# Kernel tuning notes

Measured on AMD Instinct MI355X. Metric: run time of the kernel, lower is better.

The kernel has to match this reference:

```python
import jax, jax.numpy as jnp
import numpy as np

B = 50000      # batch of graphs
NOBJ = 7       # tangram pieces per graph
HID = 64
EMB = 32
SIGMA = 25.0   # VE-SDE sigma for marginal_prob_std


def _lin_init(k, fin, fout):
    kw, kb = jax.random.split(k)
    s = 1.0 / np.sqrt(fin)
    w = jax.random.uniform(kw, (fin, fout), minval=-s, maxval=s, dtype=jnp.float32)
    b = jax.random.uniform(kb, (fout,), minval=-s, maxval=s, dtype=jnp.float32)
    return w, b


def setup_inputs() -> dict:
    key = jax.random.key(0)
    ks = jax.random.split(key, 16)
    N = B * NOBJ
    omega = jax.random.normal(ks[0], (N, 3), dtype=jnp.float32)
    t = jax.random.uniform(ks[1], (B, 1), minval=1e-3, maxval=1.0, dtype=jnp.float32)
    # fully-connected edges (no self loops) per graph, offset by graph index
    a, b = np.meshgrid(np.arange(NOBJ), np.arange(NOBJ), indexing='ij')
    m = a != b
    src0, dst0 = a[m], b[m]                       # (42,)
    offs = (np.arange(B) * NOBJ)[:, None]         # (B,1)
    src = (src0[None, :] + offs).reshape(-1)
    dst = (dst0[None, :] + offs).reshape(-1)
    edge_index = jnp.asarray(np.stack([src, dst]), dtype=jnp.int32)  # (2, B*42)
    W_fourier = jax.random.normal(ks[2], (EMB // 2,), dtype=jnp.float32) * 30.0
    wi1, bi1 = _lin_init(ks[3], 3, HID)
    wi2, bi2 = _lin_init(ks[4], HID, HID)
    wt, bt = _lin_init(ks[5], EMB, EMB)
    w1a, b1a = _lin_init(ks[6], HID * 2, HID)
    w1b, b1b = _lin_init(ks[7], HID, HID)
    w2a, b2a = _lin_init(ks[8], (HID + EMB) * 2, HID)
    w2b, b2b = _lin_init(ks[9], HID, HID)
    w3a, b3a = _lin_init(ks[10], (HID + EMB) * 2, HID)
    w3b, b3b = _lin_init(ks[11], HID, 3)
    return dict(omega=omega, edge_index=edge_index, t=t, num_objs=NOBJ,
                W_fourier=W_fourier,
                wi1=wi1, bi1=bi1, wi2=wi2, bi2=bi2, wt=wt, bt=bt,
                w1a=w1a, b1a=b1a, w1b=w1b, b1b=b1b,
                w2a=w2a, b2a=b2a, w2b=w2b, b2b=b2b,
                w3a=w3a, b3a=b3a, w3b=w3b, b3b=b3b)


def _mlp(x, wa, ba, wb, bb):
    return jax.nn.relu(x @ wa + ba) @ wb + bb


def reference(omega, edge_index, t, num_objs, W_fourier,
              wi1, bi1, wi2, bi2, wt, bt,
              w1a, b1a, w1b, b1b, w2a, b2a, w2b, b2b, w3a, b3a, w3b, b3b):
    N = omega.shape[0]
    src, dst = edge_index[0], edge_index[1]

    def edge_conv(x, wa, ba, wb, bb):
        # EdgeConv: msg = mlp([x_i, x_j - x_i]); max-aggregate at target i
        xi = x[dst]
        msg = _mlp(jnp.concatenate([xi, x[src] - xi], axis=-1), wa, ba, wb, bb)
        return jax.ops.segment_max(msg, dst, num_segments=N)

    init_feature = _mlp(omega, wi1, bi1, wi2, bi2)          # (N, HID)
    # Gaussian Fourier time embedding -> ReLU -> Linear -> ReLU
    proj = t[:, 0][:, None] * W_fourier[None, :] * (2.0 * jnp.pi)   # (B, EMB/2)
    emb = jnp.concatenate([jnp.sin(proj), jnp.cos(proj)], axis=-1)  # (B, EMB)
    xs = jax.nn.relu(jax.nn.relu(emb) @ wt + bt)                    # (B, EMB)
    # torch: xs.repeat(1, num_objs, 1).view(B*num_objs, -1) == tile whole block
    x_sigma = jnp.tile(xs, (num_objs, 1))                           # (N, EMB)

    x = jax.nn.relu(edge_conv(init_feature, w1a, b1a, w1b, b1b))
    x = jnp.concatenate([x, x_sigma], axis=-1)
    x = jax.nn.relu(edge_conv(x, w2a, b2a, w2b, b2b))
    x = jnp.concatenate([x, x_sigma], axis=-1)
    x = edge_conv(x, w3a, b3a, w3b, b3b)                            # (N, 3)

    # torch: t.repeat(1, num_objs).view(B*num_objs, -1) == repeat_interleave
    t_r = jnp.repeat(t, num_objs, axis=0)                           # (N, 1)
    std = jnp.sqrt((SIGMA ** (2.0 * t_r) - 1.0) / (2.0 * jnp.log(SIGMA)))
    return x / (std + 1e-7)
```

## Files before the change

### kernel.cpp

```cpp
#include <hip/hip_runtime.h>


#define NB 50000

typedef unsigned short u16;
typedef unsigned int u32;
typedef short short8 __attribute__((ext_vector_type(8)));
typedef float f32x4 __attribute__((ext_vector_type(4)));

#define OFF_I  0
#define OFF_1A 8192
#define OFF_2A 24576
#define OFF_3A 49152
#define OFF_1B 73728
#define OFF_2B 81920
#define OFF_WT 90112
#define OFF_3B 92160

#define HSTR 144
#define HLO  2304
#define H2S  272
#define SSTR 264
#define WREG 8832

__device__ __forceinline__ float b2f(u16 u) {
    return __uint_as_float(((u32)u) << 16);
}
__device__ __forceinline__ u16 f2b(float f) {
    u32 u = __float_as_uint(f);
    u += 0x7FFFu + ((u >> 16) & 1u);
    return (u16)(u >> 16);
}
__device__ __forceinline__ void split2(float v, u16& h, u16& l) {
    u32 u = __float_as_uint(v);
    h = (u16)(u >> 16);
    float d = v - __uint_as_float(u & 0xffff0000u);
    l = f2b(d);
}
__device__ __forceinline__ u32 splitpack(float v) {
    u32 u = __float_as_uint(v);
    float d = v - __uint_as_float(u & 0xffff0000u);
    u32 r = __float_as_uint(d);
    r += 0x7FFFu + ((r >> 16) & 1u);
    return __builtin_amdgcn_perm(r, u, 0x07060302);
}
__device__ __forceinline__ float bcast(float v, int l) {
    return __uint_as_float(__builtin_amdgcn_readlane(__float_as_uint(v), l));
}

__global__ __launch_bounds__(128) void pack_kernel(
    const float* __restrict__ wi2, const float* __restrict__ w1a,
    const float* __restrict__ w2a, const float* __restrict__ w3a,
    const float* __restrict__ w1b, const float* __restrict__ w2b,
    const float* __restrict__ wt,  const float* __restrict__ w3b,
    u16* __restrict__ ws)
{
    int blk = blockIdx.x;
    int j    = blockIdx.y;
    int half = threadIdx.x >> 6;
    int lane = threadIdx.x & 63;
    float v;
    u16* dst;
    if (blk < 88) {
        const float* src; int NT, qoff, obase, frag;
        if (blk < 8)       { src = wi2; NT = 4; qoff = 0;  obase = OFF_I;  frag = blk;      }
        else if (blk < 24) { src = w1a; NT = 8; qoff = 64; obase = OFF_1A; frag = blk - 8;  }
        else if (blk < 48) { src = w2a; NT = 8; qoff = 96; obase = OFF_2A; frag = blk - 24; }
        else if (blk < 72) { src = w3a; NT = 8; qoff = 96; obase = OFF_3A; frag = blk - 48; }
        else if (blk < 80) { src = w1b; NT = 4; qoff = 0;  obase = OFF_1B; frag = blk - 72; }
        else               { src = w2b; NT = 4; qoff = 0;  obase = OFF_2B; frag = blk - 80; }
        int kt = frag / NT, nt = frag % NT;
        int k = kt * 32 + (lane >> 4) * 8 + j;
        int n = nt * 16 + (lane & 15);
        int idx = (n < 64) ? (k * 64 + n) : ((qoff + k) * 64 + (n - 64));
        v = src[idx];
        dst = ws + obase + frag * 1024 + half * 512 + lane * 8 + j;
    } else if (blk < 90) {
        int frag = blk - 88;
        int k = (lane >> 4) * 8 + j;
        int n = frag * 16 + (lane & 15);
        v = wt[k * 32 + n];
        dst = ws + OFF_WT + frag * 1024 + half * 512 + lane * 8 + j;
    } else {
        int frag = blk - 90;
        int k = frag * 32 + (lane >> 4) * 8 + j;
        int n = lane & 15;
        v = (n < 3) ? w3b[k * 3 + n] : 0.f;
        dst = ws + OFF_3B + frag * 1024 + half * 512 + lane * 8 + j;
    }
    u16 hi = f2b(v);
    *dst = (half == 0) ? hi : f2b(v - b2f(hi));
}

__device__ __forceinline__ f32x4 mfma1(short8 a, short8 b, f32x4 acc) {
    return __builtin_amdgcn_mfma_f32_16x16x32_bf16(a, b, acc, 0, 0, 0);
}
__device__ __forceinline__ f32x4 mfma3(short8 ah, short8 al, short8 bh, short8 bl, f32x4 acc) {
    acc = mfma1(ah, bh, acc);
    acc = mfma1(ah, bl, acc);
    acc = mfma1(al, bh, acc);
    return acc;
}

#define ROW(k) ((k) < 7 ? (k) : (k) + 1)

__device__ __forceinline__ void writeX64_14(char* G, int L, const float* v) {
#pragma unroll
    for (int k = 0; k < 14; ++k) {
        int r = ROW(k);
        u16 h, l;
        split2(v[k], h, l);
        *(u16*)(G + r * HSTR + L * 2) = h;
        *(u16*)(G + HLO + r * HSTR + L * 2) = l;
    }
}
__device__ __forceinline__ void loadA2(const char* G, int L, short8* Ah, short8* Al) {
#pragma unroll
    for (int kt = 0; kt < 2; ++kt) {
        Ah[kt] = *(const short8*)(G + (L & 15) * HSTR + kt * 64 + (L >> 4) * 16);
        Al[kt] = *(const short8*)(G + HLO + (L & 15) * HSTR + kt * 64 + (L >> 4) * 16);
    }
}
template<int KT, int NT>
__device__ __forceinline__ void lin_pass(const u16* __restrict__ ws, int off, int nt0,
                                         const short8* Ah, const short8* Al,
                                         char* Sg, int L) {
#pragma unroll
    for (int ntc = 0; ntc < 4; ++ntc) {
        f32x4 a1 = {0.f, 0.f, 0.f, 0.f}, a2 = {0.f, 0.f, 0.f, 0.f};
#pragma unroll
        for (int kt = 0; kt < KT; ++kt) {
            int f = kt * NT + nt0 + ntc;
            short8 bh = *(const short8*)(ws + off + f * 1024 + L * 8);
            short8 bl = *(const short8*)(ws + off + f * 1024 + 512 + L * 8);
            a1 = mfma1(Ah[kt], bh, a1);
            a2 = mfma1(Ah[kt], bl, a2);
            a2 = mfma1(Al[kt], bh, a2);
        }
#pragma unroll
        for (int rr = 0; rr < 4; ++rr)
            *(float*)(Sg + ((L >> 4) * 4 + rr) * SSTR + ntc * 64 + (L & 15) * 4) = a1[rr] + a2[rr];
    }
}
__device__ __forceinline__ void readS14(const char* Sg, int L, float* o) {
#pragma unroll
    for (int k = 0; k < 14; ++k) o[k] = *(const float*)(Sg + ROW(k) * SSTR + L * 4);
}
__device__ __forceinline__ void stageH2(char* G, int c, const float* pp, const float* qq, int L) {
#pragma unroll
    for (int r = 0; r < 16; ++r) {
        int e = c * 16 + r;
        if (e < 84) {
            int gb = (e >= 42) ? 1 : 0;
            int el = e - gb * 42;
            int i = el / 6, jj = el - i * 6;
            int j = jj + (jj >= i);
            float hv = fmaxf(pp[gb * 7 + i] + qq[gb * 7 + j], 0.f);
            *(u32*)(G + r * H2S + L * 4) = splitpack(hv);
        }
    }
}
__device__ __forceinline__ void unpack4(const uint4& a, u32* ho, u32* lo) {
    ho[0] = __builtin_amdgcn_perm(a.y, a.x, 0x05040100);
    ho[1] = __builtin_amdgcn_perm(a.w, a.z, 0x05040100);
    lo[0] = __builtin_amdgcn_perm(a.y, a.x, 0x07060302);
    lo[1] = __builtin_amdgcn_perm(a.w, a.z, 0x07060302);
}
__device__ __forceinline__ void loadAH(const char* G, int L,
                                       short8& Ah0, short8& Ah1, short8& Al0, short8& Al1) {
    const char* base = G + (L & 15) * H2S + (L >> 4) * 32;
    uint4 a0 = *(const uint4*)(base);
    uint4 a1 = *(const uint4*)(base + 16);
    uint4 b0 = *(const uint4*)(base + 128);
    uint4 b1 = *(const uint4*)(base + 144);
    union { u32 u[4]; short8 s; } h0, h1, l0, l1;
    unpack4(a0, &h0.u[0], &l0.u[0]);
    unpack4(a1, &h0.u[2], &l0.u[2]);
    unpack4(b0, &h1.u[0], &l1.u[0]);
    unpack4(b1, &h1.u[2], &l1.u[2]);
    Ah0 = h0.s; Al0 = l0.s; Ah1 = h1.s; Al1 = l1.s;
}
__device__ __forceinline__ void maxread(const char* Sb, int cc, float* mx, int L) {
#pragma unroll
    for (int r = 0; r < 16; ++r) {
        int e = cc * 16 + r;
        if (e < 84) {
            int gb = (e >= 42) ? 1 : 0;
            int i = (e - gb * 42) / 6;
            float sv = *(const float*)(Sb + r * SSTR + L * 4);
            mx[gb * 7 + i] = fmaxf(mx[gb * 7 + i], sv);
        }
    }
}

__device__ __forceinline__ void edgeconv_pipe(const u16* __restrict__ ws, int offB,
                                              char* W, char* Sb,
                                              const float* pp, const float* qq,
                                              float vb, int L) {
    float mx[14];
#pragma unroll
    for (int k = 0; k < 14; ++k) mx[k] = -3.0e38f;
    stageH2(W, 0, pp, qq, L);
    short8 Ah0, Ah1, Al0, Al1;
    loadAH(W, L, Ah0, Ah1, Al0, Al1);
#pragma unroll
    for (int c = 0; c < 6; ++c) {
        if (c < 5) stageH2(W, c + 1, pp, qq, L);
        if (c > 0) maxread(Sb, c - 1, mx, L);
#pragma unroll
        for (int nt = 0; nt < 4; ++nt) {
            short8 bh0 = *(const short8*)(ws + offB + nt * 1024 + L * 8);
            short8 bl0 = *(const short8*)(ws + offB + nt * 1024 + 512 + L * 8);
            short8 bh1 = *(const short8*)(ws + offB + (4 + nt) * 1024 + L * 8);
            short8 bl1 = *(const short8*)(ws + offB + (4 + nt) * 1024 + 512 + L * 8);
            f32x4 a1 = {0.f, 0.f, 0.f, 0.f}, a2 = {0.f, 0.f, 0.f, 0.f};
            a1 = mfma1(Ah0, bh0, a1);
            a2 = mfma1(Ah0, bl0, a2);
            a2 = mfma1(Al0, bh0, a2);
            a1 = mfma1(Ah1, bh1, a1);
            a2 = mfma1(Ah1, bl1, a2);
            a2 = mfma1(Al1, bh1, a2);
#pragma unroll
            for (int rr = 0; rr < 4; ++rr)
                *(float*)(Sb + ((L >> 4) * 4 + rr) * SSTR + nt * 64 + (L & 15) * 4) = a1[rr] + a2[rr];
        }
        if (c < 5) loadAH(W, L, Ah0, Ah1, Al0, Al1);
    }
    maxread(Sb, 5, mx, L);
    float xo[14];
#pragma unroll
    for (int k = 0; k < 14; ++k) xo[k] = fmaxf(mx[k] + vb, 0.f);
    writeX64_14(W, L, xo);
}

__global__ __launch_bounds__(128, 3) void gnn_kernel(
    const float* __restrict__ omega, const float* __restrict__ tt, const float* __restrict__ Wf,
    const float* __restrict__ wi1, const float* __restrict__ bi1, const float* __restrict__ bi2,
    const float* __restrict__ bt,
    const float* __restrict__ b1a, const float* __restrict__ b1b,
    const float* __restrict__ b2a, const float* __restrict__ b2b,
    const float* __restrict__ b3a, const float* __restrict__ b3b,
    const u16* __restrict__ ws, float* __restrict__ out)
{
    __shared__ __align__(16) char smem[2 * WREG];
    const int L   = threadIdx.x & 63;
    const int wav = threadIdx.x >> 6;
    const int p   = blockIdx.x * 2 + wav;
    const int g0  = p * 2;
    const int base0 = g0 * 7;
    char* W   = smem + wav * WREG;
    char* Sb  = W + 4608;

    float omv = (L < 42) ? omega[base0 * 3 + L] : 0.f;
    float vwi10 = wi1[L], vwi11 = wi1[64 + L], vwi12 = wi1[128 + L];
    float vbi1 = bi1[L];
    float h1[14];
#pragma unroll
    for (int k = 0; k < 14; ++k) {
        float a0 = bcast(omv, 3 * k), a1 = bcast(omv, 3 * k + 1), a2 = bcast(omv, 3 * k + 2);
        h1[k] = fmaxf(fmaf(a0, vwi10, fmaf(a1, vwi11, fmaf(a2, vwi12, vbi1))), 0.f);
    }

    short8 Ah2, Al2;
    {
        int cc = L & 31;
        float vwf = Wf[cc & 15] * 6.283185307179586f;
        int tb = base0 - (base0 / NB) * NB;
#pragma unroll
        for (int k = 0; k < 14; ++k) {
            int ti = tb + k; if (ti >= NB) ti -= NB;
            float pj = tt[ti] * vwf;
            float remb = fmaxf((cc < 16) ? __sinf(pj) : __cosf(pj), 0.f);
            u16 h, l;
            split2(remb, h, l);
            if (L < 32) *(u16*)(W + ROW(k) * HSTR + cc * 2) = h;
            else *(u16*)(W + HLO + ROW(k) * HSTR + cc * 2) = l;
        }
        short8 Eh = *(const short8*)(W + (L & 15) * HSTR + (L >> 4) * 16);
        short8 El = *(const short8*)(W + HLO + (L & 15) * HSTR + (L >> 4) * 16);
#pragma unroll
        for (int nt = 0; nt < 2; ++nt) {
            short8 bh = *(const short8*)(ws + OFF_WT + nt * 1024 + L * 8);
            short8 bl = *(const short8*)(ws + OFF_WT + nt * 1024 + 512 + L * 8);
            f32x4 acc = {0.f, 0.f, 0.f, 0.f};
            acc = mfma3(Eh, El, bh, bl, acc);
#pragma unroll
            for (int rr = 0; rr < 4; ++rr)
                *(float*)(Sb + ((L >> 4) * 4 + rr) * SSTR + nt * 64 + (L & 15) * 4) = acc[rr];
        }
        float vbt = bt[cc];
#pragma unroll
        for (int k = 0; k < 14; ++k) {
            float xv = fmaxf(*(const float*)(Sb + ROW(k) * SSTR + cc * 4) + vbt, 0.f);
            u16 h, l;
            split2(xv, h, l);
            if (L < 32) *(u16*)(W + ROW(k) * HSTR + cc * 2) = h;
            else *(u16*)(W + HLO + ROW(k) * HSTR + cc * 2) = l;
        }
        Ah2 = *(const short8*)(W + (L & 15) * HSTR + (L >> 4) * 16);
        Al2 = *(const short8*)(W + HLO + (L & 15) * HSTR + (L >> 4) * 16);
    }

    short8 Ah[3], Al[3];
    float pp[14], qq[14];

    writeX64_14(W, L, h1);
    loadA2(W, L, Ah, Al);
    lin_pass<2, 4>(ws, OFF_I, 0, Ah, Al, Sb, L);
    {
        float xh[14];
        readS14(Sb, L, xh);
        float vbi2 = bi2[L];
#pragma unroll
        for (int k = 0; k < 14; ++k) xh[k] += vbi2;
        writeX64_14(W, L, xh);
    }

    loadA2(W, L, Ah, Al);
    lin_pass<2, 8>(ws, OFF_1A, 0, Ah, Al, Sb, L);
    readS14(Sb, L, pp);
    lin_pass<2, 8>(ws, OFF_1A, 4, Ah, Al, Sb, L);
    readS14(Sb, L, qq);
    float vb1a = b1a[L];
#pragma unroll
    for (int k = 0; k < 14; ++k) pp[k] = pp[k] + vb1a - qq[k];
    edgeconv_pipe(ws, OFF_1B, W, Sb, pp, qq, b1b[L], L);

    loadA2(W, L, Ah, Al);
    Ah[2] = Ah2; Al[2] = Al2;
    lin_pass<3, 8>(ws, OFF_2A, 0, Ah, Al, Sb, L);
    readS14(Sb, L, pp);
    lin_pass<3, 8>(ws, OFF_2A, 4, Ah, Al, Sb, L);
    readS14(Sb, L, qq);
    float vb2a = b2a[L];
#pragma unroll
    for (int k = 0; k < 14; ++k) pp[k] = pp[k] + vb2a - qq[k];
    edgeconv_pipe(ws, OFF_2B, W, Sb, pp, qq, b2b[L], L);

    loadA2(W, L, Ah, Al);
    Ah[2] = Ah2; Al[2] = Al2;
    lin_pass<3, 8>(ws, OFF_3A, 0, Ah, Al, Sb, L);
    readS14(Sb, L, pp);
    lin_pass<3, 8>(ws, OFF_3A, 4, Ah, Al, Sb, L);
    readS14(Sb, L, qq);
    float vb3a = b3a[L];
#pragma unroll
    for (int k = 0; k < 14; ++k) pp[k] = pp[k] + vb3a - qq[k];

    {
        short8 B0h = *(const short8*)(ws + OFF_3B + L * 8);
        short8 B0l = *(const short8*)(ws + OFF_3B + 512 + L * 8);
        short8 B1h = *(const short8*)(ws + OFF_3B + 1024 + L * 8);
        short8 B1l = *(const short8*)(ws + OFF_3B + 1536 + L * 8);
        stageH2(W, 0, pp, qq, L);
        short8 Ah0, Ah1, Al0, Al1;
        loadAH(W, L, Ah0, Ah1, Al0, Al1);
#pragma unroll
        for (int c = 0; c < 6; ++c) {
            if (c < 5) stageH2(W, c + 1, pp, qq, L);
            f32x4 a1 = {0.f, 0.f, 0.f, 0.f}, a2 = {0.f, 0.f, 0.f, 0.f};
            a1 = mfma1(Ah0, B0h, a1);
            a2 = mfma1(Ah0, B0l, a2);
            a2 = mfma1(Al0, B0h, a2);
            a1 = mfma1(Ah1, B1h, a1);
            a2 = mfma1(Ah1, B1l, a2);
            a2 = mfma1(Al1, B1h, a2);
            if ((L & 15) < 3) {
#pragma unroll
                for (int rr = 0; rr < 4; ++rr)
                    *(float*)(Sb + (c * 16 + (L >> 4) * 4 + rr) * 16 + (L & 15) * 4) = a1[rr] + a2[rr];
            }
            if (c < 5) loadAH(W, L, Ah0, Ah1, Al0, Al1);
        }
        if (L < 42) {
            int gb = (L >= 21) ? 1 : 0;
            int ll = L - gb * 21;
            int i = ll / 3, col = ll - i * 3;
            int e0 = gb * 42 + i * 6;
            float m = -3.0e38f;
#pragma unroll
            for (int e6 = 0; e6 < 6; ++e6)
                m = fmaxf(m, *(const float*)(Sb + (e0 + e6) * 16 + col * 4));
            m += b3b[col];
            float tg = tt[g0 + gb];
            float stdv = sqrtf((exp2f(tg * 9.287712379549448f) - 1.0f) * 0.15533740282828987f);
            out[base0 * 3 + L] = m / (stdv + 1e-7f);
        }
    }
}

extern "C" void kernel_launch(void* const* d_in, const int* in_sizes, int n_in,
                              void* d_out, int out_size, void* d_ws, size_t ws_size,
                              hipStream_t stream) {
    const float* omega = (const float*)d_in[0];
    const float* tt  = (const float*)d_in[2];
    const float* Wf  = (const float*)d_in[4];
    const float* wi1 = (const float*)d_in[5];
    const float* bi1 = (const float*)d_in[6];
    const float* wi2 = (const float*)d_in[7];
    const float* bi2 = (const float*)d_in[8];
    const float* wt  = (const float*)d_in[9];
    const float* bt  = (const float*)d_in[10];
    const float* w1a = (const float*)d_in[11];
    const float* b1a = (const float*)d_in[12];
    const float* w1b = (const float*)d_in[13];
    const float* b1b = (const float*)d_in[14];
    const float* w2a = (const float*)d_in[15];
    const float* b2a = (const float*)d_in[16];
    const float* w2b = (const float*)d_in[17];
    const float* b2b = (const float*)d_in[18];
    const float* w3a = (const float*)d_in[19];
    const float* b3a = (const float*)d_in[20];
    const float* w3b = (const float*)d_in[21];
    const float* b3b = (const float*)d_in[22];
    u16* ws = (u16*)d_ws;

    pack_kernel<<<dim3(92, 8), dim3(128), 0, stream>>>(wi2, w1a, w2a, w3a, w1b, w2b, wt, w3b, ws);
    gnn_kernel<<<dim3(12500), dim3(128), 0, stream>>>(
        omega, tt, Wf, wi1, bi1, bi2, bt,
        b1a, b1b, b2a, b2b, b3a, b3b, ws, (float*)d_out);
}
```

Measured before the change: 415.4 us.

## Build edge-MLP A fragments directly from staged P/Q rows in LDS

Instead of each lane computing all 84 edge hidden vectors and writing packed hi/lo bf16 pairs to LDS, the per-node P and Q vectors are written once to LDS (28 rows). Each lane then gathers its edge's p_i and q_j rows and forms the relu sum plus hi/lo bf16 split in registers, using a packed bf16 convert instruction. This removes the redundant per-chunk staging writes and most of the conversion work, but enlarges per-wave LDS from 8832 to 12288 bytes, which may reduce occupancy, and adds more LDS reads per fragment.

```diff
diff --git a/kernel.cpp b/kernel.cpp
--- a/kernel.cpp
+++ b/kernel.cpp
@@ -19,9 +19,10 @@
 
 #define HSTR 144
 #define HLO  2304
-#define H2S  272
+#define PQS  288
+#define SOFF 8064
 #define SSTR 264
-#define WREG 8832
+#define WREG 12288
 
 __device__ __forceinline__ float b2f(u16 u) {
     return __uint_as_float(((u32)u) << 16);
@@ -36,13 +37,6 @@
     h = (u16)(u >> 16);
     float d = v - __uint_as_float(u & 0xffff0000u);
     l = f2b(d);
-}
-__device__ __forceinline__ u32 splitpack(float v) {
-    u32 u = __float_as_uint(v);
-    float d = v - __uint_as_float(u & 0xffff0000u);
-    u32 r = __float_as_uint(d);
-    r += 0x7FFFu + ((r >> 16) & 1u);
-    return __builtin_amdgcn_perm(r, u, 0x07060302);
 }
 __device__ __forceinline__ float bcast(float v, int l) {
     return __uint_as_float(__builtin_amdgcn_readlane(__float_as_uint(v), l));
@@ -146,39 +140,49 @@
 #pragma unroll
     for (int k = 0; k < 14; ++k) o[k] = *(const float*)(Sg + ROW(k) * SSTR + L * 4);
 }
-__device__ __forceinline__ void stageH2(char* G, int c, const float* pp, const float* qq, int L) {
-#pragma unroll
-    for (int r = 0; r < 16; ++r) {
-        int e = c * 16 + r;
-        if (e < 84) {
-            int gb = (e >= 42) ? 1 : 0;
-            int el = e - gb * 42;
-            int i = el / 6, jj = el - i * 6;
-            int j = jj + (jj >= i);
-            float hv = fmaxf(pp[gb * 7 + i] + qq[gb * 7 + j], 0.f);
-            *(u32*)(G + r * H2S + L * 4) = splitpack(hv);
-        }
-    }
-}
-__device__ __forceinline__ void unpack4(const uint4& a, u32* ho, u32* lo) {
-    ho[0] = __builtin_amdgcn_perm(a.y, a.x, 0x05040100);
-    ho[1] = __builtin_amdgcn_perm(a.w, a.z, 0x05040100);
-    lo[0] = __builtin_amdgcn_perm(a.y, a.x, 0x07060302);
-    lo[1] = __builtin_amdgcn_perm(a.w, a.z, 0x07060302);
-}
-__device__ __forceinline__ void loadAH(const char* G, int L,
-                                       short8& Ah0, short8& Ah1, short8& Al0, short8& Al1) {
-    const char* base = G + (L & 15) * H2S + (L >> 4) * 32;
-    uint4 a0 = *(const uint4*)(base);
-    uint4 a1 = *(const uint4*)(base + 16);
-    uint4 b0 = *(const uint4*)(base + 128);
-    uint4 b1 = *(const uint4*)(base + 144);
-    union { u32 u[4]; short8 s; } h0, h1, l0, l1;
-    unpack4(a0, &h0.u[0], &l0.u[0]);
-    unpack4(a1, &h0.u[2], &l0.u[2]);
-    unpack4(b0, &h1.u[0], &l1.u[0]);
-    unpack4(b1, &h1.u[2], &l1.u[2]);
-    Ah0 = h0.s; Al0 = l0.s; Ah1 = h1.s; Al1 = l1.s;
+__device__ __forceinline__ void writePQ(char* PQ, int L, const float* pp, const float* qq) {
+#pragma unroll
+    for (int k = 0; k < 14; ++k) {
+        *(float*)(PQ + k * PQS + L * 4) = pp[k];
+        *(float*)(PQ + (14 + k) * PQS + L * 4) = qq[k];
+    }
+}
+__device__ __forceinline__ void buildA1(const char* bp, const char* bq,
+                                        short8& Ah, short8& Al) {
+    f32x4 p0 = *(const f32x4*)bp,  p1 = *(const f32x4*)(bp + 16);
+    f32x4 q0 = *(const f32x4*)bq,  q1 = *(const f32x4*)(bq + 16);
+    float h[8];
+#pragma unroll
+    for (int x = 0; x < 4; ++x) h[x]     = fmaxf(p0[x] + q0[x], 0.f);
+#pragma unroll
+    for (int x = 0; x < 4; ++x) h[4 + x] = fmaxf(p1[x] + q1[x], 0.f);
+    union { u32 u[4]; short8 s; } H, Lo;
+#pragma unroll
+    for (int x = 0; x < 4; ++x) {
+        float a = h[2 * x], b = h[2 * x + 1];
+        u32 ua = __float_as_uint(a), ub = __float_as_uint(b);
+        H.u[x] = __builtin_amdgcn_perm(ub, ua, 0x07060302);
+        float da = a - __uint_as_float(ua & 0xffff0000u);
+        float db = b - __uint_as_float(ub & 0xffff0000u);
+        u32 r;
+        asm("v_cvt_pk_bf16_f32 %0, %1, %2" : "=v"(r) : "v"(da), "v"(db));
+        Lo.u[x] = r;
+    }
+    Ah = H.s; Al = Lo.s;
+}
+__device__ __forceinline__ void buildA(const char* PQ, int c, int L,
+                                       short8& Ah0, short8& Al0,
+                                       short8& Ah1, short8& Al1) {
+    int e  = c * 16 + (L & 15);
+    int gb = (e >= 42) ? 1 : 0;
+    int el = e - gb * 42;
+    int i  = el / 6;
+    int jj = el - i * 6;
+    int j  = jj + (jj >= i);
+    const char* bp = PQ + (gb * 7 + i) * PQS + (L >> 4) * 32;
+    const char* bq = PQ + (14 + gb * 7 + j) * PQS + (L >> 4) * 32;
+    buildA1(bp,       bq,       Ah0, Al0);
+    buildA1(bp + 128, bq + 128, Ah1, Al1);
 }
 __device__ __forceinline__ void maxread(const char* Sb, int cc, float* mx, int L) {
 #pragma unroll
@@ -194,18 +198,15 @@
 }
 
 __device__ __forceinline__ void edgeconv_pipe(const u16* __restrict__ ws, int offB,
-                                              char* W, char* Sb,
-                                              const float* pp, const float* qq,
-                                              float vb, int L) {
+                                              char* W, char* Sb, float vb, int L) {
+    const char* PQ = W;
     float mx[14];
 #pragma unroll
     for (int k = 0; k < 14; ++k) mx[k] = -3.0e38f;
-    stageH2(W, 0, pp, qq, L);
     short8 Ah0, Ah1, Al0, Al1;
-    loadAH(W, L, Ah0, Ah1, Al0, Al1);
+    buildA(PQ, 0, L, Ah0, Al0, Ah1, Al1);
 #pragma unroll
     for (int c = 0; c < 6; ++c) {
-        if (c < 5) stageH2(W, c + 1, pp, qq, L);
         if (c > 0) maxread(Sb, c - 1, mx, L);
 #pragma unroll
         for (int nt = 0; nt < 4; ++nt) {
@@ -224,7 +225,7 @@
             for (int rr = 0; rr < 4; ++rr)
                 *(float*)(Sb + ((L >> 4) * 4 + rr) * SSTR + nt * 64 + (L & 15) * 4) = a1[rr] + a2[rr];
         }
-        if (c < 5) loadAH(W, L, Ah0, Ah1, Al0, Al1);
+        if (c < 5) buildA(PQ, c + 1, L, Ah0, Al0, Ah1, Al1);
     }
     maxread(Sb, 5, mx, L);
     float xo[14];
@@ -249,7 +250,7 @@
     const int g0  = p * 2;
     const int base0 = g0 * 7;
     char* W   = smem + wav * WREG;
-    char* Sb  = W + 4608;
+    char* Sb  = W + SOFF;
 
     float omv = (L < 42) ? omega[base0 * 3 + L] : 0.f;
     float vwi10 = wi1[L], vwi11 = wi1[64 + L], vwi12 = wi1[128 + L];
@@ -302,7 +303,6 @@
     }
 
     short8 Ah[3], Al[3];
-    float pp[14], qq[14];
 
     writeX64_14(W, L, h1);
     loadA2(W, L, Ah, Al);
@@ -316,48 +316,59 @@
         writeX64_14(W, L, xh);
     }
 
-    loadA2(W, L, Ah, Al);
-    lin_pass<2, 8>(ws, OFF_1A, 0, Ah, Al, Sb, L);
-    readS14(Sb, L, pp);
-    lin_pass<2, 8>(ws, OFF_1A, 4, Ah, Al, Sb, L);
-    readS14(Sb, L, qq);
-    float vb1a = b1a[L];
-#pragma unroll
-    for (int k = 0; k < 14; ++k) pp[k] = pp[k] + vb1a - qq[k];
-    edgeconv_pipe(ws, OFF_1B, W, Sb, pp, qq, b1b[L], L);
-
-    loadA2(W, L, Ah, Al);
-    Ah[2] = Ah2; Al[2] = Al2;
-    lin_pass<3, 8>(ws, OFF_2A, 0, Ah, Al, Sb, L);
-    readS14(Sb, L, pp);
-    lin_pass<3, 8>(ws, OFF_2A, 4, Ah, Al, Sb, L);
-    readS14(Sb, L, qq);
-    float vb2a = b2a[L];
-#pragma unroll
-    for (int k = 0; k < 14; ++k) pp[k] = pp[k] + vb2a - qq[k];
-    edgeconv_pipe(ws, OFF_2B, W, Sb, pp, qq, b2b[L], L);
-
-    loadA2(W, L, Ah, Al);
-    Ah[2] = Ah2; Al[2] = Al2;
-    lin_pass<3, 8>(ws, OFF_3A, 0, Ah, Al, Sb, L);
-    readS14(Sb, L, pp);
-    lin_pass<3, 8>(ws, OFF_3A, 4, Ah, Al, Sb, L);
-    readS14(Sb, L, qq);
-    float vb3a = b3a[L];
-#pragma unroll
-    for (int k = 0; k < 14; ++k) pp[k] = pp[k] + vb3a - qq[k];
-
-    {
+    {
+        float pp[14], qq[14];
+        loadA2(W, L, Ah, Al);
+        lin_pass<2, 8>(ws, OFF_1A, 0, Ah, Al, Sb, L);
+        readS14(Sb, L, pp);
+        lin_pass<2, 8>(ws, OFF_1A, 4, Ah, Al, Sb, L);
+        readS14(Sb, L, qq);
+        float vb = b1a[L];
+#pragma unroll
+        for (int k = 0; k < 14; ++k) pp[k] = pp[k] + vb - qq[k];
+        writePQ(W, L, pp, qq);
+    }
+    edgeconv_pipe(ws, OFF_1B, W, Sb, b1b[L], L);
+
+    {
+        float pp[14], qq[14];
+        loadA2(W, L, Ah, Al);
+        Ah[2] = Ah2; Al[2] = Al2;
+        lin_pass<3, 8>(ws, OFF_2A, 0, Ah, Al, Sb, L);
+        readS14(Sb, L, pp);
+        lin_pass<3, 8>(ws, OFF_2A, 4, Ah, Al, Sb, L);
+        readS14(Sb, L, qq);
+        float vb = b2a[L];
+#pragma unroll
+        for (int k = 0; k < 14; ++k) pp[k] = pp[k] + vb - qq[k];
+        writePQ(W, L, pp, qq);
+    }
+    edgeconv_pipe(ws, OFF_2B, W, Sb, b2b[L], L);
+
+    {
+        float pp[14], qq[14];
+        loadA2(W, L, Ah, Al);
+        Ah[2] = Ah2; Al[2] = Al2;
+        lin_pass<3, 8>(ws, OFF_3A, 0, Ah, Al, Sb, L);
+        readS14(Sb, L, pp);
+        lin_pass<3, 8>(ws, OFF_3A, 4, Ah, Al, Sb, L);
+        readS14(Sb, L, qq);
+        float vb = b3a[L];
+#pragma unroll
+        for (int k = 0; k < 14; ++k) pp[k] = pp[k] + vb - qq[k];
+        writePQ(W, L, pp, qq);
+    }
+
+    {
+        const char* PQ = W;
         short8 B0h = *(const short8*)(ws + OFF_3B + L * 8);
         short8 B0l = *(const short8*)(ws + OFF_3B + 512 + L * 8);
         short8 B1h = *(const short8*)(ws + OFF_3B + 1024 + L * 8);
         short8 B1l = *(const short8*)(ws + OFF_3B + 1536 + L * 8);
-        stageH2(W, 0, pp, qq, L);
         short8 Ah0, Ah1, Al0, Al1;
-        loadAH(W, L, Ah0, Ah1, Al0, Al1);
+        buildA(PQ, 0, L, Ah0, Al0, Ah1, Al1);
 #pragma unroll
         for (int c = 0; c < 6; ++c) {
-            if (c < 5) stageH2(W, c + 1, pp, qq, L);
             f32x4 a1 = {0.f, 0.f, 0.f, 0.f}, a2 = {0.f, 0.f, 0.f, 0.f};
             a1 = mfma1(Ah0, B0h, a1);
             a2 = mfma1(Ah0, B0l, a2);
@@ -370,7 +381,7 @@
                 for (int rr = 0; rr < 4; ++rr)
                     *(float*)(Sb + (c * 16 + (L >> 4) * 4 + rr) * 16 + (L & 15) * 4) = a1[rr] + a2[rr];
             }
-            if (c < 5) loadAH(W, L, Ah0, Ah1, Al0, Al1);
+            if (c < 5) buildA(PQ, c + 1, L, Ah0, Al0, Ah1, Al1);
         }
         if (L < 42) {
             int gb = (L >= 21) ? 1 : 0;
```

Measured after the change: 400.1 us. 1.04x faster.
